# Performance work log

Hardware: AMD Instinct MI355X
Metric: run time of the kernel (lower is better)

## Reference

```python
import jax, jax.numpy as jnp
import numpy as np

N_HEAD = 16


def setup_inputs() -> dict:
    key = jax.random.key(0)
    k1, k2, k3 = jax.random.split(key, 3)
    B, T, C = 4, 2048, 2048
    x = jax.random.normal(k1, (B, T, C), dtype=jnp.float32)
    # weights stored as [in, out] so y = x @ W + b (equivalent to torch Linear)
    w_attn = jax.random.normal(k2, (C, 3 * C), dtype=jnp.float32) * 0.02
    b_attn = jnp.zeros((3 * C,), dtype=jnp.float32)
    w_proj = jax.random.normal(k3, (C, C), dtype=jnp.float32) * 0.02
    b_proj = jnp.zeros((C,), dtype=jnp.float32)
    return {"x": x, "w_attn": w_attn, "b_attn": b_attn, "w_proj": w_proj, "b_proj": b_proj}


def reference(x, w_attn, b_attn, w_proj, b_proj):
    B, T, C = x.shape
    H = N_HEAD
    D = C // H
    qkv = x @ w_attn + b_attn                     # [B,T,3C]
    q, k, v = jnp.split(qkv, 3, axis=-1)
    q = q.reshape(B, T, H, D).transpose(0, 2, 1, 3)  # [B,H,T,D]
    k = k.reshape(B, T, H, D).transpose(0, 2, 1, 3)
    v = v.reshape(B, T, H, D).transpose(0, 2, 1, 3)
    att = jnp.einsum("bhqd,bhkd->bhqk", q, k) * (1.0 / jnp.sqrt(jnp.float32(D)))
    causal = jnp.tril(jnp.ones((T, T), dtype=bool))
    att = jnp.where(causal[None, None], att, jnp.float32(-jnp.inf))
    att = jax.nn.softmax(att, axis=-1)
    y = jnp.einsum("bhqk,bhkd->bhqd", att, v)     # [B,H,T,D]
    y = y.transpose(0, 2, 1, 3).reshape(B, T, C)
    return y @ w_proj + b_proj
```

## Files before the change

kernel.cpp:

```cpp
#include <hip/hip_runtime.h>
#include <cstdint>

typedef unsigned short u16;
typedef u16   u16x8 __attribute__((ext_vector_type(8)));
typedef short s16x8 __attribute__((ext_vector_type(8)));
typedef float f32x4 __attribute__((ext_vector_type(4)));

__device__ __forceinline__ u16 f2bf(float f) {
  union { float f; unsigned u; } v; v.f = f;
  unsigned u = v.u;
  return (u16)((u + 0x7fffu + ((u >> 16) & 1u)) >> 16);
}

__device__ __forceinline__ void gld_lds16(const u16* g, u16* l) {
  __builtin_amdgcn_global_load_lds((const __attribute__((address_space(1))) void*)g,
                                   (__attribute__((address_space(3))) void*)l, 16, 0, 0);
}

__global__ void cast_f32_bf16_k(const float* __restrict__ in, u16* __restrict__ out) {
  size_t i = ((size_t)blockIdx.x * 256 + threadIdx.x) * 8;
  float4 a = *(const float4*)(in + i);
  float4 b = *(const float4*)(in + i + 4);
  u16x8 r;
  r[0] = f2bf(a.x); r[1] = f2bf(a.y); r[2] = f2bf(a.z); r[3] = f2bf(a.w);
  r[4] = f2bf(b.x); r[5] = f2bf(b.y); r[6] = f2bf(b.z); r[7] = f2bf(b.w);
  *(u16x8*)(out + i) = r;
}

__global__ void transpose_cast_f32_k(const float* __restrict__ in, u16* __restrict__ outp,
                                     int R, int Cin) {
  __shared__ u16 tile[64][72];
  const int c0 = blockIdx.x * 64, r0 = blockIdx.y * 64;
  const int t = threadIdx.x;
  const int r = t >> 2, cs = (t & 3) * 16;
  const float* src = in + (size_t)(r0 + r) * Cin + c0 + cs;
#pragma unroll
  for (int q = 0; q < 4; ++q) {
    float4 v = *(const float4*)(src + q * 4);
    tile[r][cs + q * 4 + 0] = f2bf(v.x);
    tile[r][cs + q * 4 + 1] = f2bf(v.y);
    tile[r][cs + q * 4 + 2] = f2bf(v.z);
    tile[r][cs + q * 4 + 3] = f2bf(v.w);
  }
  __syncthreads();
  u16x8 w0, w1;
#pragma unroll
  for (int q = 0; q < 8; ++q) { w0[q] = tile[cs + q][r]; w1[q] = tile[cs + 8 + q][r]; }
  u16* dst = outp + (size_t)(c0 + r) * R + r0 + cs;
  *(u16x8*)dst = w0;
  *(u16x8*)(dst + 8) = w1;
}

__global__ void transpose_v_k(const u16* __restrict__ V, u16* __restrict__ Vt) {
  __shared__ u16 tile[64][72];
  const int t0 = blockIdx.x * 64, d0 = blockIdx.y * 64, bh = blockIdx.z;
  const int t = threadIdx.x;
  const int r = t >> 2, cs = (t & 3) * 16;
  const u16* src = V + ((size_t)bh * 2048 + t0 + r) * 128 + d0 + cs;
  u16x8 a0 = *(const u16x8*)src;
  u16x8 a1 = *(const u16x8*)(src + 8);
#pragma unroll
  for (int q = 0; q < 8; ++q) { tile[r][cs + q] = a0[q]; tile[r][cs + 8 + q] = a1[q]; }
  __syncthreads();
  u16x8 w0, w1;
#pragma unroll
  for (int q = 0; q < 8; ++q) { w0[q] = tile[cs + q][r]; w1[q] = tile[cs + 8 + q][r]; }
  u16* dst = Vt + ((size_t)bh * 128 + d0 + r) * 2048 + t0 + cs;
  *(u16x8*)dst = w0;
  *(u16x8*)(dst + 8) = w1;
}

template <int EPI>
__global__ __launch_bounds__(512, 2) void gemm256(
    const u16* __restrict__ A, const u16* __restrict__ Bt,
    const float* __restrict__ bias,
    u16* __restrict__ o0, u16* __restrict__ o1, u16* __restrict__ o2,
    float* __restrict__ ofp, int Ntiles, int Kdim) {
  __shared__ __align__(128) u16 sm[65536];
  const int nwg = gridDim.x;
  const int orig = blockIdx.x;
  const int qq = nwg >> 3;
  const int bid = (orig & 7) * qq + (orig >> 3);
  const int mt = bid / Ntiles, nt = bid % Ntiles;
  const int tid = threadIdx.x, lane = tid & 63, wave = tid >> 6;
  const int wr = wave >> 2, wc = wave & 3;
  const int l15 = lane & 15, lhi = lane >> 4;
  f32x4 acc[8][4] = {};
  const int nK = Kdim >> 6;

#define VMA(n) asm volatile("s_waitcnt vmcnt(" #n ")" ::: "memory")
#define BARK   asm volatile("s_barrier" ::: "memory")
#define LG0                                                   \
  do {                                                        \
    asm volatile("s_waitcnt lgkmcnt(0)" ::: "memory");        \
    __builtin_amdgcn_sched_barrier(0);                        \
  } while (0)
#define DSA(qm)                                                                          \
  do {                                                                                   \
    _Pragma("unroll") for (int mi = 0; mi < 4; ++mi)                                     \
    _Pragma("unroll") for (int kk = 0; kk < 2; ++kk)                                     \
      af[mi * 2 + kk] = *(const s16x8*)&sm[(size_t)(cA + (qm) * 1024 +                   \
          (kk * 4 + lhi) * 128 + wr * 64 + mi * 16 + l15) * 8];                          \
  } while (0)
#define DSB(qn)                                                                          \
  do {                                                                                   \
    _Pragma("unroll") for (int ni = 0; ni < 2; ++ni)                                     \
    _Pragma("unroll") for (int kk = 0; kk < 2; ++kk)                                     \
      bf[ni * 2 + kk] = *(const s16x8*)&sm[(size_t)(cB + (qn) * 1024 +                   \
          (kk * 4 + lhi) * 128 + wc * 32 + ni * 16 + l15) * 8];                          \
  } while (0)
#define STA(qm, k0, sbase)                                                               \
  do {                                                                                   \
    _Pragma("unroll") for (int l = 0; l < 2; ++l)                                        \
      gld_lds16(A + (size_t)(mt * 256 + (wave & 1) * 128 + (qm) * 64 + lane) * Kdim +    \
                    (k0) + (l * 4 + (wave >> 1)) * 8,                                    \
                &sm[(size_t)((sbase) + (qm) * 1024 + l * 512 + wave * 64) * 8]);         \
  } while (0)
#define STB(qn, k0, sbase)                                                               \
  do {                                                                                   \
    _Pragma("unroll") for (int l = 0; l < 2; ++l)                                        \
      gld_lds16(Bt + (size_t)(nt * 256 + ((wave & 1) * 2 + (lane >> 5)) * 64 +           \
                              (qn) * 32 + (lane & 31)) * Kdim +                          \
                     (k0) + (l * 4 + (wave >> 1)) * 8,                                   \
                &sm[(size_t)((sbase) + (qn) * 1024 + l * 512 + wave * 64) * 8]);         \
  } while (0)
#define MM(qm, qn)                                                                       \
  do {                                                                                   \
    __builtin_amdgcn_s_setprio(1);                                                       \
    _Pragma("unroll") for (int mi = 0; mi < 4; ++mi)                                     \
    _Pragma("unroll") for (int ni = 0; ni < 2; ++ni)                                     \
    _Pragma("unroll") for (int kk = 0; kk < 2; ++kk)                                     \
      acc[(qm) * 4 + mi][(qn) * 2 + ni] = __builtin_amdgcn_mfma_f32_16x16x32_bf16(       \
          af[mi * 2 + kk], bf[ni * 2 + kk], acc[(qm) * 4 + mi][(qn) * 2 + ni], 0, 0, 0); \
    __builtin_amdgcn_s_setprio(0);                                                       \
  } while (0)

  STA(0, 0, 0); STB(0, 0, 4096); STB(1, 0, 4096); STA(1, 0, 0);
  VMA(4);
  BARK;

  for (int t = 0; t < nK; ++t) {
    const int cA = (t & 1) * 2048, cB = 4096 + (t & 1) * 2048;
    const int sA = ((t & 1) ^ 1) * 2048, sB = 4096 + ((t & 1) ^ 1) * 2048;
    const int k1 = (t + 1) << 6;
    const bool st = (t + 1 < nK);
    s16x8 af[8], bf[4];
    DSA(0); DSB(0);
    if (st) { STA(0, k1, sA); VMA(4); } else { VMA(2); }
    BARK; LG0; MM(0, 0); BARK;
    DSB(1);
    if (st) { STB(0, k1, sB); VMA(4); } else { VMA(0); }
    BARK; LG0; MM(0, 1); BARK;
    DSA(1);
    if (st) STB(1, k1, sB);
    BARK; LG0; MM(1, 1); BARK;
    DSB(0);
    if (st) { STA(1, k1, sA); VMA(4); }
    BARK; LG0; MM(1, 0); BARK;
  }
#undef VMA
#undef BARK
#undef LG0
#undef DSA
#undef DSB
#undef STA
#undef STB
#undef MM

  const int row0 = mt * 256 + wr * 128;
  const int col0 = nt * 256 + wc * 64;
  float bcol[4];
#pragma unroll
  for (int ni = 0; ni < 4; ++ni) bcol[ni] = bias[col0 + ni * 16 + l15];
  if constexpr (EPI == 0) {
#pragma unroll
    for (int ni = 0; ni < 4; ++ni) {
      int cc = col0 + ni * 16 + l15;
      int which = cc >> 11, h = (cc >> 7) & 15, d = cc & 127;
      u16* o = (which == 0) ? o0 : (which == 1) ? o1 : o2;
#pragma unroll
      for (int mi = 0; mi < 8; ++mi)
#pragma unroll
        for (int j = 0; j < 4; ++j) {
          int row = row0 + mi * 16 + lhi * 4 + j;
          int bb = row >> 11, tt = row & 2047;
          o[(((size_t)bb * 16 + h) * 2048 + tt) * 128 + d] = f2bf(acc[mi][ni][j] + bcol[ni]);
        }
    }
  } else {
#pragma unroll
    for (int mi = 0; mi < 8; ++mi)
#pragma unroll
      for (int j = 0; j < 4; ++j) {
        int row = row0 + mi * 16 + lhi * 4 + j;
#pragma unroll
        for (int ni = 0; ni < 4; ++ni)
          ofp[(size_t)row * 2048 + col0 + ni * 16 + l15] = acc[mi][ni][j] + bcol[ni];
      }
  }
}

__global__ __launch_bounds__(512, 4) void attn_k(
    const u16* __restrict__ Q, const u16* __restrict__ Kg,
    const u16* __restrict__ Vt, u16* __restrict__ Y) {
  __shared__ u16 Ks[8192];
  __shared__ u16 Vs[8192];
  __shared__ u16 Ps[8][16 * 72];
  const int p = blockIdx.x, bh = blockIdx.y;
  const int tid = threadIdx.x, lane = tid & 63, wave = tid >> 6;
  const int l15 = lane & 15, lhi = lane >> 4;
  const size_t bhT = (size_t)bh * 2048;
  const int b = bh >> 4, h = bh & 15;
  const float sc = 0.08838834764831845f * 1.4426950408889634f;

  for (int hf = 0; hf < 2; ++hf) {
    const int qt = hf ? 15 - p : p;
    const int r0 = qt * 128 + wave * 16;
    const int last = 2 * qt + 1;

    s16x8 qf[4];
#pragma unroll
    for (int kk = 0; kk < 4; ++kk)
      qf[kk] = *(const s16x8*)&Q[(bhT + r0 + l15) * 128 + kk * 32 + lhi * 8];

    f32x4 o[8] = {};
    float m_[4], l_[4];
#pragma unroll
    for (int j = 0; j < 4; ++j) { m_[j] = -1e30f; l_[j] = 0.f; }

    __syncthreads();
#pragma unroll
    for (int c = 0; c < 2; ++c) {
      int ci = c * 512 + tid;
      int dhi = ci >> 6, key = ci & 63;
      gld_lds16(Kg + (bhT + key) * 128 + dhi * 8, &Ks[(c * 512 + wave * 64) * 8]);
      int khi = ci >> 7, d = ci & 127;
      gld_lds16(Vt + ((size_t)bh * 128 + d) * 2048 + khi * 8, &Vs[(c * 512 + wave * 64) * 8]);
    }
    __syncthreads();

    for (int it = 0; it <= last; ++it) {
      const int j0 = it * 64;
      const bool have_next = (it < last);
      u16x8 kpre[2], vpre[2];
      if (have_next) {
        const int j1 = j0 + 64;
#pragma unroll
        for (int c = 0; c < 2; ++c) {
          int ci = c * 512 + tid;
          int dhi = ci >> 6, key = ci & 63;
          kpre[c] = *(const u16x8*)&Kg[(bhT + j1 + key) * 128 + dhi * 8];
          int khi = ci >> 7, d = ci & 127;
          vpre[c] = *(const u16x8*)&Vt[((size_t)bh * 128 + d) * 2048 + j1 + khi * 8];
        }
      }

      if (j0 <= r0 + 15) {
        f32x4 s[4] = {};
#pragma unroll
        for (int nc = 0; nc < 4; ++nc)
#pragma unroll
          for (int kk = 0; kk < 4; ++kk) {
            s16x8 kf = *(const s16x8*)&Ks[((kk * 4 + lhi) * 64 + nc * 16 + l15) * 8];
            s[nc] = __builtin_amdgcn_mfma_f32_16x16x32_bf16(qf[kk], kf, s[nc], 0, 0, 0);
          }
        const bool maskt = (j0 + 63 > r0);
        float rmax[4];
#pragma unroll
        for (int j = 0; j < 4; ++j) rmax[j] = -1e30f;
#pragma unroll
        for (int nc = 0; nc < 4; ++nc)
#pragma unroll
          for (int j = 0; j < 4; ++j) {
            float v = s[nc][j] * sc;
            if (maskt && (j0 + nc * 16 + l15) > (r0 + lhi * 4 + j)) v = -1e30f;
            s[nc][j] = v;
            rmax[j] = fmaxf(rmax[j], v);
          }
#pragma unroll
        for (int off = 1; off < 16; off <<= 1)
#pragma unroll
          for (int j = 0; j < 4; ++j) rmax[j] = fmaxf(rmax[j], __shfl_xor(rmax[j], off));

        float al[4], rsum[4];
#pragma unroll
        for (int j = 0; j < 4; ++j) {
          float mn = fmaxf(m_[j], rmax[j]);
          al[j] = exp2f(m_[j] - mn);
          m_[j] = mn;
          rsum[j] = 0.f;
        }
#pragma unroll
        for (int nc = 0; nc < 4; ++nc)
#pragma unroll
          for (int j = 0; j < 4; ++j) {
            float pv = exp2f(s[nc][j] - m_[j]);
            rsum[j] += pv;
            Ps[wave][(lhi * 4 + j) * 72 + nc * 16 + l15] = f2bf(pv);
          }
#pragma unroll
        for (int off = 1; off < 16; off <<= 1)
#pragma unroll
          for (int j = 0; j < 4; ++j) rsum[j] += __shfl_xor(rsum[j], off);
#pragma unroll
        for (int j = 0; j < 4; ++j) l_[j] = l_[j] * al[j] + rsum[j];
#pragma unroll
        for (int di = 0; di < 8; ++di)
#pragma unroll
          for (int j = 0; j < 4; ++j) o[di][j] *= al[j];

#pragma unroll
        for (int kk2 = 0; kk2 < 2; ++kk2) {
          s16x8 pf = *(const s16x8*)&Ps[wave][l15 * 72 + kk2 * 32 + lhi * 8];
#pragma unroll
          for (int di = 0; di < 8; ++di) {
            s16x8 vf = *(const s16x8*)&Vs[((kk2 * 4 + lhi) * 128 + di * 16 + l15) * 8];
            o[di] = __builtin_amdgcn_mfma_f32_16x16x32_bf16(pf, vf, o[di], 0, 0, 0);
          }
        }
      }

      if (have_next) {
        __syncthreads();
#pragma unroll
        for (int c = 0; c < 2; ++c) {
          *(u16x8*)&Ks[(c * 512 + tid) * 8] = kpre[c];
          *(u16x8*)&Vs[(c * 512 + tid) * 8] = vpre[c];
        }
        __syncthreads();
      }
    }

    float rl[4];
#pragma unroll
    for (int j = 0; j < 4; ++j) rl[j] = 1.0f / l_[j];
#pragma unroll
    for (int di = 0; di < 8; ++di)
#pragma unroll
      for (int j = 0; j < 4; ++j) {
        int row = b * 2048 + r0 + lhi * 4 + j;
        int col = h * 128 + di * 16 + l15;
        Y[(size_t)row * 2048 + col] = f2bf(o[di][j] * rl[j]);
      }
  }
}

extern "C" void kernel_launch(void* const* d_in, const int* in_sizes, int n_in,
                              void* d_out, int out_size, void* d_ws, size_t ws_size,
                              hipStream_t stream) {
  const float* x      = (const float*)d_in[0];
  const float* w_attn = (const float*)d_in[1];
  const float* b_attn = (const float*)d_in[2];
  const float* w_proj = (const float*)d_in[3];
  const float* b_proj = (const float*)d_in[4];
  float* out = (float*)d_out;

  char* ws = (char*)d_ws;
  u16* xb  = (u16*)(ws);
  u16* waT = (u16*)(ws + 33554432ull);
  u16* wpT = (u16*)(ws + 58720256ull);
  u16* Qb  = (u16*)(ws + 67108864ull);
  u16* Kb  = (u16*)(ws + 100663296ull);
  u16* Vb  = (u16*)(ws + 134217728ull);
  u16* Vtb = (u16*)(ws + 167772160ull);
  u16* Yb  = xb;

  cast_f32_bf16_k<<<8192, 256, 0, stream>>>(x, xb);
  transpose_cast_f32_k<<<dim3(96, 32), 256, 0, stream>>>(w_attn, waT, 2048, 6144);
  transpose_cast_f32_k<<<dim3(32, 32), 256, 0, stream>>>(w_proj, wpT, 2048, 2048);
  gemm256<0><<<32 * 24, 512, 0, stream>>>(xb, waT, b_attn, Qb, Kb, Vb, nullptr, 24, 2048);
  transpose_v_k<<<dim3(32, 2, 64), 256, 0, stream>>>(Vb, Vtb);
  attn_k<<<dim3(8, 64), 512, 0, stream>>>(Qb, Kb, Vtb, Yb);
  gemm256<1><<<32 * 8, 512, 0, stream>>>(Yb, wpT, b_proj, nullptr, nullptr, nullptr, out, 8, 2048);
}
```

Measured before the change: 584.2 us.

## Restructure GEMM main loop into 4-stage K=32 pipeline with one barrier per step

Replaces the double-buffered K=64 loop, which used four quadrant phases and many barriers, with a 4-slot ring of K=32 sub-tiles prefetched three steps ahead. Each step has a single barrier and issues the global-to-LDS loads for step s+3 while it computes. The goal is to cut barrier and sync overhead and hide more memory latency. The trade-off is fewer MFMAs per barrier, a different LDS layout that may bank-conflict, and tighter vmcnt accounting. Running the last two steps with no prefetch leaves an unusual wait count to check.

Measured after the change: 658.7 us. 1.13x slower.

```diff
diff --git a/kernel.cpp b/kernel.cpp
--- a/kernel.cpp
+++ b/kernel.cpp
@@ -86,86 +86,82 @@
   const int wr = wave >> 2, wc = wave & 3;
   const int l15 = lane & 15, lhi = lane >> 4;
   f32x4 acc[8][4] = {};
-  const int nK = Kdim >> 6;
-
-#define VMA(n) asm volatile("s_waitcnt vmcnt(" #n ")" ::: "memory")
-#define BARK   asm volatile("s_barrier" ::: "memory")
-#define LG0                                                   \
+  const int nS = Kdim >> 5;
+
+#define LGKM0                                                 \
   do {                                                        \
     asm volatile("s_waitcnt lgkmcnt(0)" ::: "memory");        \
     __builtin_amdgcn_sched_barrier(0);                        \
   } while (0)
-#define DSA(qm)                                                                          \
-  do {                                                                                   \
-    _Pragma("unroll") for (int mi = 0; mi < 4; ++mi)                                     \
-    _Pragma("unroll") for (int kk = 0; kk < 2; ++kk)                                     \
-      af[mi * 2 + kk] = *(const s16x8*)&sm[(size_t)(cA + (qm) * 1024 +                   \
-          (kk * 4 + lhi) * 128 + wr * 64 + mi * 16 + l15) * 8];                          \
-  } while (0)
-#define DSB(qn)                                                                          \
-  do {                                                                                   \
-    _Pragma("unroll") for (int ni = 0; ni < 2; ++ni)                                     \
-    _Pragma("unroll") for (int kk = 0; kk < 2; ++kk)                                     \
-      bf[ni * 2 + kk] = *(const s16x8*)&sm[(size_t)(cB + (qn) * 1024 +                   \
-          (kk * 4 + lhi) * 128 + wc * 32 + ni * 16 + l15) * 8];                          \
-  } while (0)
-#define STA(qm, k0, sbase)                                                               \
-  do {                                                                                   \
-    _Pragma("unroll") for (int l = 0; l < 2; ++l)                                        \
-      gld_lds16(A + (size_t)(mt * 256 + (wave & 1) * 128 + (qm) * 64 + lane) * Kdim +    \
-                    (k0) + (l * 4 + (wave >> 1)) * 8,                                    \
-                &sm[(size_t)((sbase) + (qm) * 1024 + l * 512 + wave * 64) * 8]);         \
-  } while (0)
-#define STB(qn, k0, sbase)                                                               \
-  do {                                                                                   \
-    _Pragma("unroll") for (int l = 0; l < 2; ++l)                                        \
-      gld_lds16(Bt + (size_t)(nt * 256 + ((wave & 1) * 2 + (lane >> 5)) * 64 +           \
-                              (qn) * 32 + (lane & 31)) * Kdim +                          \
-                     (k0) + (l * 4 + (wave >> 1)) * 8,                                   \
-                &sm[(size_t)((sbase) + (qn) * 1024 + l * 512 + wave * 64) * 8]);         \
-  } while (0)
-#define MM(qm, qn)                                                                       \
+#define STAGEA(t)                                                             \
+  do {                                                                        \
+    const int tb_ = (t) & 3;                                                  \
+    _Pragma("unroll") for (int j = 0; j < 2; ++j) {                           \
+      int ci = j * 512 + tid;                                                 \
+      int row = ci & 255, khi = ci >> 8;                                      \
+      gld_lds16(A + (size_t)(mt * 256 + row) * Kdim + (t) * 32 + khi * 8,     \
+                &sm[(size_t)(tb_ * 2048 + j * 512 + wave * 64) * 8]);         \
+    }                                                                         \
+  } while (0)
+#define STAGEB(t)                                                             \
+  do {                                                                        \
+    const int tb_ = (t) & 3;                                                  \
+    _Pragma("unroll") for (int j = 0; j < 2; ++j) {                           \
+      int ci = j * 512 + tid;                                                 \
+      int row = ci & 255, khi = ci >> 8;                                      \
+      gld_lds16(Bt + (size_t)(nt * 256 + row) * Kdim + (t) * 32 + khi * 8,    \
+                &sm[(size_t)(tb_ * 2048 + 1024 + j * 512 + wave * 64) * 8]);  \
+    }                                                                         \
+  } while (0)
+#define LDA(cb, hm, mi) \
+  (*(const s16x8*)&sm[((cb) + lhi * 256 + wr * 128 + (hm) * 64 + (mi) * 16 + l15) * 8])
+#define LDB(cb, ni) \
+  (*(const s16x8*)&sm[((cb) + 1024 + lhi * 256 + wc * 64 + (ni) * 16 + l15) * 8])
+#define MFMAROW(base, a0, a1, a2, a3)                                                    \
   do {                                                                                   \
     __builtin_amdgcn_s_setprio(1);                                                       \
-    _Pragma("unroll") for (int mi = 0; mi < 4; ++mi)                                     \
-    _Pragma("unroll") for (int ni = 0; ni < 2; ++ni)                                     \
-    _Pragma("unroll") for (int kk = 0; kk < 2; ++kk)                                     \
-      acc[(qm) * 4 + mi][(qn) * 2 + ni] = __builtin_amdgcn_mfma_f32_16x16x32_bf16(       \
-          af[mi * 2 + kk], bf[ni * 2 + kk], acc[(qm) * 4 + mi][(qn) * 2 + ni], 0, 0, 0); \
+    _Pragma("unroll") for (int ni = 0; ni < 4; ++ni) {                                   \
+      s16x8 bfx = (ni == 0) ? bf0 : (ni == 1) ? bf1 : (ni == 2) ? bf2 : bf3;             \
+      acc[(base) + 0][ni] = __builtin_amdgcn_mfma_f32_16x16x32_bf16(a0, bfx, acc[(base) + 0][ni], 0, 0, 0); \
+      acc[(base) + 1][ni] = __builtin_amdgcn_mfma_f32_16x16x32_bf16(a1, bfx, acc[(base) + 1][ni], 0, 0, 0); \
+      acc[(base) + 2][ni] = __builtin_amdgcn_mfma_f32_16x16x32_bf16(a2, bfx, acc[(base) + 2][ni], 0, 0, 0); \
+      acc[(base) + 3][ni] = __builtin_amdgcn_mfma_f32_16x16x32_bf16(a3, bfx, acc[(base) + 3][ni], 0, 0, 0); \
+    }                                                                                    \
     __builtin_amdgcn_s_setprio(0);                                                       \
   } while (0)
-
-  STA(0, 0, 0); STB(0, 0, 4096); STB(1, 0, 4096); STA(1, 0, 0);
-  VMA(4);
-  BARK;
-
-  for (int t = 0; t < nK; ++t) {
-    const int cA = (t & 1) * 2048, cB = 4096 + (t & 1) * 2048;
-    const int sA = ((t & 1) ^ 1) * 2048, sB = 4096 + ((t & 1) ^ 1) * 2048;
-    const int k1 = (t + 1) << 6;
-    const bool st = (t + 1 < nK);
-    s16x8 af[8], bf[4];
-    DSA(0); DSB(0);
-    if (st) { STA(0, k1, sA); VMA(4); } else { VMA(2); }
-    BARK; LG0; MM(0, 0); BARK;
-    DSB(1);
-    if (st) { STB(0, k1, sB); VMA(4); } else { VMA(0); }
-    BARK; LG0; MM(0, 1); BARK;
-    DSA(1);
-    if (st) STB(1, k1, sB);
-    BARK; LG0; MM(1, 1); BARK;
-    DSB(0);
-    if (st) { STA(1, k1, sA); VMA(4); }
-    BARK; LG0; MM(1, 0); BARK;
-  }
-#undef VMA
-#undef BARK
-#undef LG0
-#undef DSA
-#undef DSB
-#undef STA
-#undef STB
-#undef MM
+#define SUBT(s, VML)                                                          \
+  do {                                                                        \
+    const size_t cb_ = (size_t)((s) & 3) * 2048;                              \
+    asm volatile("s_waitcnt vmcnt(" VML ")" ::: "memory");                    \
+    __builtin_amdgcn_s_barrier();                                             \
+    asm volatile("" ::: "memory");                                            \
+    if ((s) + 3 < nS) STAGEA((s) + 3);                                        \
+    s16x8 af0 = LDA(cb_, 0, 0), af1 = LDA(cb_, 0, 1);                         \
+    s16x8 af2 = LDA(cb_, 0, 2), af3 = LDA(cb_, 0, 3);                         \
+    s16x8 bf0 = LDB(cb_, 0), bf1 = LDB(cb_, 1);                               \
+    s16x8 bf2 = LDB(cb_, 2), bf3 = LDB(cb_, 3);                               \
+    LGKM0;                                                                    \
+    MFMAROW(0, af0, af1, af2, af3);                                           \
+    if ((s) + 3 < nS) STAGEB((s) + 3);                                        \
+    af0 = LDA(cb_, 1, 0); af1 = LDA(cb_, 1, 1);                               \
+    af2 = LDA(cb_, 1, 2); af3 = LDA(cb_, 1, 3);                               \
+    LGKM0;                                                                    \
+    MFMAROW(4, af0, af1, af2, af3);                                           \
+  } while (0)
+
+  STAGEA(0); STAGEB(0); STAGEA(1); STAGEB(1); STAGEA(2); STAGEB(2);
+
+  for (int s = 0; s < nS - 2; ++s) SUBT(s, "8");
+  SUBT(nS - 2, "4");
+  SUBT(nS - 1, "0");
+
+#undef LGKM0
+#undef STAGEA
+#undef STAGEB
+#undef LDA
+#undef LDB
+#undef MFMAROW
+#undef SUBT
 
   const int row0 = mt * 256 + wr * 128;
   const int col0 = nt * 256 + wc * 64;
```

## Merge prep casts into one kernel and write V transposed from QKV GEMM epilogue

Applied to the files above, without the earlier changes.

Folds the three input-cast and weight-transpose kernels into one launch that picks its work by block index. The QKV GEMM epilogue now writes the V slice directly in [B,H,D,T] layout using 4-element vector stores, which removes the separate V transpose kernel and its round trip through memory. The cost is strided 8-byte stores for V in the epilogue instead of per-element stores to a contiguous layout.

Result: faster. 557.4 us (-4.6%).

```diff
diff --git a/kernel.cpp b/kernel.cpp
--- a/kernel.cpp
+++ b/kernel.cpp
@@ -2,6 +2,7 @@
 #include <cstdint>
 
 typedef unsigned short u16;
+typedef u16   u16x4 __attribute__((ext_vector_type(4)));
 typedef u16   u16x8 __attribute__((ext_vector_type(8)));
 typedef short s16x8 __attribute__((ext_vector_type(8)));
 typedef float f32x4 __attribute__((ext_vector_type(4)));
@@ -17,20 +18,10 @@
                                    (__attribute__((address_space(3))) void*)l, 16, 0, 0);
 }
 
-__global__ void cast_f32_bf16_k(const float* __restrict__ in, u16* __restrict__ out) {
-  size_t i = ((size_t)blockIdx.x * 256 + threadIdx.x) * 8;
-  float4 a = *(const float4*)(in + i);
-  float4 b = *(const float4*)(in + i + 4);
-  u16x8 r;
-  r[0] = f2bf(a.x); r[1] = f2bf(a.y); r[2] = f2bf(a.z); r[3] = f2bf(a.w);
-  r[4] = f2bf(b.x); r[5] = f2bf(b.y); r[6] = f2bf(b.z); r[7] = f2bf(b.w);
-  *(u16x8*)(out + i) = r;
-}
-
-__global__ void transpose_cast_f32_k(const float* __restrict__ in, u16* __restrict__ outp,
-                                     int R, int Cin) {
-  __shared__ u16 tile[64][72];
-  const int c0 = blockIdx.x * 64, r0 = blockIdx.y * 64;
+__device__ __forceinline__ void transpose_cast_body(
+    const float* __restrict__ in, u16* __restrict__ outp, int R, int Cin,
+    int cx, int cy, u16 (*tile)[72]) {
+  const int c0 = cx * 64, r0 = cy * 64;
   const int t = threadIdx.x;
   const int r = t >> 2, cs = (t & 3) * 16;
   const float* src = in + (size_t)(r0 + r) * Cin + c0 + cs;
@@ -51,23 +42,26 @@
   *(u16x8*)(dst + 8) = w1;
 }
 
-__global__ void transpose_v_k(const u16* __restrict__ V, u16* __restrict__ Vt) {
+__global__ void prep_k(const float* __restrict__ x, u16* __restrict__ xb,
+                       const float* __restrict__ w_attn, u16* __restrict__ waT,
+                       const float* __restrict__ w_proj, u16* __restrict__ wpT) {
   __shared__ u16 tile[64][72];
-  const int t0 = blockIdx.x * 64, d0 = blockIdx.y * 64, bh = blockIdx.z;
-  const int t = threadIdx.x;
-  const int r = t >> 2, cs = (t & 3) * 16;
-  const u16* src = V + ((size_t)bh * 2048 + t0 + r) * 128 + d0 + cs;
-  u16x8 a0 = *(const u16x8*)src;
-  u16x8 a1 = *(const u16x8*)(src + 8);
-#pragma unroll
-  for (int q = 0; q < 8; ++q) { tile[r][cs + q] = a0[q]; tile[r][cs + 8 + q] = a1[q]; }
-  __syncthreads();
-  u16x8 w0, w1;
-#pragma unroll
-  for (int q = 0; q < 8; ++q) { w0[q] = tile[cs + q][r]; w1[q] = tile[cs + 8 + q][r]; }
-  u16* dst = Vt + ((size_t)bh * 128 + d0 + r) * 2048 + t0 + cs;
-  *(u16x8*)dst = w0;
-  *(u16x8*)(dst + 8) = w1;
+  const int bx = blockIdx.x;
+  if (bx < 8192) {
+    size_t i = ((size_t)bx * 256 + threadIdx.x) * 8;
+    float4 a = *(const float4*)(x + i);
+    float4 b = *(const float4*)(x + i + 4);
+    u16x8 r;
+    r[0] = f2bf(a.x); r[1] = f2bf(a.y); r[2] = f2bf(a.z); r[3] = f2bf(a.w);
+    r[4] = f2bf(b.x); r[5] = f2bf(b.y); r[6] = f2bf(b.z); r[7] = f2bf(b.w);
+    *(u16x8*)(xb + i) = r;
+  } else if (bx < 11264) {
+    int idx = bx - 8192;
+    transpose_cast_body(w_attn, waT, 2048, 6144, idx % 96, idx / 96, tile);
+  } else {
+    int idx = bx - 11264;
+    transpose_cast_body(w_proj, wpT, 2048, 2048, idx % 32, idx / 32, tile);
+  }
 }
 
 template <int EPI>
@@ -177,15 +171,27 @@
     for (int ni = 0; ni < 4; ++ni) {
       int cc = col0 + ni * 16 + l15;
       int which = cc >> 11, h = (cc >> 7) & 15, d = cc & 127;
-      u16* o = (which == 0) ? o0 : (which == 1) ? o1 : o2;
-#pragma unroll
-      for (int mi = 0; mi < 8; ++mi)
-#pragma unroll
-        for (int j = 0; j < 4; ++j) {
-          int row = row0 + mi * 16 + lhi * 4 + j;
-          int bb = row >> 11, tt = row & 2047;
-          o[(((size_t)bb * 16 + h) * 2048 + tt) * 128 + d] = f2bf(acc[mi][ni][j] + bcol[ni]);
-        }
+      if (which == 2) {
+#pragma unroll
+        for (int mi = 0; mi < 8; ++mi) {
+          int t0 = row0 + mi * 16 + lhi * 4;
+          int bb = t0 >> 11, tt = t0 & 2047;
+          u16x4 w;
+#pragma unroll
+          for (int j = 0; j < 4; ++j) w[j] = f2bf(acc[mi][ni][j] + bcol[ni]);
+          *(u16x4*)&o2[(((size_t)bb * 16 + h) * 128 + d) * 2048 + tt] = w;
+        }
+      } else {
+        u16* o = (which == 0) ? o0 : o1;
+#pragma unroll
+        for (int mi = 0; mi < 8; ++mi)
+#pragma unroll
+          for (int j = 0; j < 4; ++j) {
+            int row = row0 + mi * 16 + lhi * 4 + j;
+            int bb = row >> 11, tt = row & 2047;
+            o[(((size_t)bb * 16 + h) * 2048 + tt) * 128 + d] = f2bf(acc[mi][ni][j] + bcol[ni]);
+          }
+      }
     }
   } else {
 #pragma unroll
@@ -361,15 +367,11 @@
   u16* wpT = (u16*)(ws + 58720256ull);
   u16* Qb  = (u16*)(ws + 67108864ull);
   u16* Kb  = (u16*)(ws + 100663296ull);
-  u16* Vb  = (u16*)(ws + 134217728ull);
   u16* Vtb = (u16*)(ws + 167772160ull);
   u16* Yb  = xb;
 
-  cast_f32_bf16_k<<<8192, 256, 0, stream>>>(x, xb);
-  transpose_cast_f32_k<<<dim3(96, 32), 256, 0, stream>>>(w_attn, waT, 2048, 6144);
-  transpose_cast_f32_k<<<dim3(32, 32), 256, 0, stream>>>(w_proj, wpT, 2048, 2048);
-  gemm256<0><<<32 * 24, 512, 0, stream>>>(xb, waT, b_attn, Qb, Kb, Vb, nullptr, 24, 2048);
-  transpose_v_k<<<dim3(32, 2, 64), 256, 0, stream>>>(Vb, Vtb);
+  prep_k<<<12288, 256, 0, stream>>>(x, xb, w_attn, waT, w_proj, wpT);
+  gemm256<0><<<32 * 24, 512, 0, stream>>>(xb, waT, b_attn, Qb, Kb, Vtb, nullptr, 24, 2048);
   attn_k<<<dim3(8, 64), 512, 0, stream>>>(Qb, Kb, Vtb, Yb);
   gemm256<1><<<32 * 8, 512, 0, stream>>>(Yb, wpT, b_proj, nullptr, nullptr, nullptr, out, 8, 2048);
 }
```
